# Kernel tuning notes

Hardware: AMD Instinct MI355X
Metric: run time of the kernel (lower is better)

Reference implementation:

```python
import jax, jax.numpy as jnp
import numpy as np

S, B, D, L = 100, 2048, 128, 2  # seq_len, batch, dim_model, n_layers
LN_EPS = 1e-5


def _layer_norm(x, g, b):
    # x: [S, B, D]; normalize over last dim (nn.LayerNorm(dim))
    mu = jnp.mean(x, axis=-1, keepdims=True)
    var = jnp.mean(jnp.square(x - mu), axis=-1, keepdims=True)
    return (x - mu) * jax.lax.rsqrt(var + LN_EPS) * g + b


def _asb(x, cw, cwh, thr):
    # Adaptive_Spectral_Block. x: [S, B, D] -> permute to [B, N, C]
    xb = jnp.transpose(x, (1, 0, 2)).astype(jnp.float32)  # [B, N, C]
    N = xb.shape[1]
    x_fft = jnp.fft.rfft(xb, axis=1, norm='ortho')  # [B, F, C] complex, F = N//2+1
    w = jax.lax.complex(cw[:, 0], cw[:, 1])          # [C]
    x_weighted = x_fft * w
    # adaptive high-frequency mask
    energy = jnp.sum(jnp.square(jnp.abs(x_fft)), axis=-1)  # [B, F]
    F = energy.shape[1]
    # torch.median returns the LOWER of the two middle values -> k-th smallest, k=(F-1)//2
    median = jnp.sort(energy, axis=1)[:, (F - 1) // 2][:, None]  # [B, 1]
    norm_e = energy / (median + 1e-6)
    threshold = jnp.quantile(norm_e, thr)  # global scalar quantile (linear interp, as torch)
    mask = (norm_e < threshold)[..., None].astype(x_fft.real.dtype)  # [B, F, 1]
    wh = jax.lax.complex(cwh[:, 0], cwh[:, 1])       # [C]
    x_weighted = x_weighted + (x_fft * mask) * wh
    out = jnp.fft.irfft(x_weighted, n=N, axis=1, norm='ortho')  # [B, N, C]
    return jnp.transpose(out, (1, 0, 2)).astype(x.dtype)  # back to [S, B, D]


def setup_inputs() -> dict:
    key = jax.random.key(0)
    k0, k1, k2, k3 = jax.random.split(key, 4)
    return {
        'x': jax.random.normal(k0, (S, B, D), dtype=jnp.float32),
        'complex_weight': jax.random.normal(k1, (L, D, 2), dtype=jnp.float32) * 0.02,
        'complex_weight_high': jax.random.normal(k2, (L, D, 2), dtype=jnp.float32) * 0.02,
        'threshold_param': jax.random.uniform(k3, (L,), dtype=jnp.float32) * 0.5,
        'gamma': jnp.ones((L, D), dtype=jnp.float32),
        'beta': jnp.zeros((L, D), dtype=jnp.float32),
    }


def reference(x, complex_weight, complex_weight_high, threshold_param, gamma, beta):
    # Encoder.forward: nlayers x (x = x + ASB(LayerNorm(x)))
    for i in range(L):
        h = _layer_norm(x, gamma[i], beta[i])
        x = x + _asb(h, complex_weight[i], complex_weight_high[i], threshold_param[i])
    return x
```

## Files before the change

kernel.cpp:

```cpp
#include <hip/hip_runtime.h>
#include <math.h>

#define SEQ    100
#define BATCH  2048
#define DIM    128
#define NF     51
#define NLAYER 2
#define MTOT   (BATCH * NF)
#define BD     (BATCH * DIM)
#define XSTR   16384

typedef __attribute__((ext_vector_type(8))) short bf16x8;
typedef __attribute__((ext_vector_type(4))) float f32x4v;

__device__ __forceinline__ unsigned short f2bf(float f) {
    unsigned u = __float_as_uint(f);
    return (unsigned short)((u + 0x7FFFu + ((u >> 16) & 1u)) >> 16);
}
__device__ __forceinline__ float bf2f(unsigned short u) {
    return __uint_as_float((unsigned)u << 16);
}

__global__ void k_tables(unsigned short* __restrict__ imgF,
                         unsigned short* __restrict__ imgI) {
    const int i = blockIdx.x * 256 + threadIdx.x;
    const float W = 6.28318530717958647692f / 100.f;
    if (i < 2 * 64 * 128) {
        const int p = i >> 13, k = (i >> 7) & 63, n = i & 127;
        float v = 0.f;
        if (k < NF && n < SEQ) {
            float s, c; sincosf((float)((k * n) % 100) * W, &s, &c);
            v = 0.1f * (p ? -s : c);
        }
        imgF[i] = f2bf(v);
    }
    if (i < 2 * 128 * 64) {
        const int p = i >> 13, n = (i >> 6) & 127, k = i & 63;
        float v = 0.f;
        if (k < NF && n < SEQ) {
            float s, c; sincosf((float)((k * n) % 100) * W, &s, &c);
            const float a = (k == 0 || k == 50) ? 0.1f : 0.2f;
            v = p ? -a * s : a * c;
        }
        imgI[i] = f2bf(v);
    }
}

__global__ __launch_bounds__(256, 4) void k_fwd(
    const float* __restrict__ x,
    const float* __restrict__ gamma, const float* __restrict__ beta,
    const unsigned short* __restrict__ imgF,
    unsigned short* __restrict__ Xg,
    float* __restrict__ normE)
{
    __shared__ __align__(16) unsigned short hT[128 * 128];
    __shared__ float epart[64][4];
    __shared__ float energy_s[64];
    __shared__ float med_s;

    const int b = blockIdx.x, t = threadIdx.x;
    const int lane = t & 63, wv = t >> 6, g4 = lane >> 4, cc = lane & 15;

    {
        const int c0 = lane * 2;
        const float2 gv = *(const float2*)&gamma[c0];
        const float2 bv = *(const float2*)&beta[c0];
        float2 v[4][8];
        #pragma unroll
        for (int slot = 0; slot < 4; ++slot) {
            const int n0 = (slot * 4 + wv) * 8;
            #pragma unroll
            for (int j = 0; j < 8; ++j)
                if (n0 + j < SEQ)
                    v[slot][j] = *(const float2*)&x[(size_t)(n0 + j) * BD + (size_t)b * DIM + c0];
        }
        #pragma unroll
        for (int slot = 0; slot < 4; ++slot) {
            const int chunk = slot * 4 + wv;
            const int n0 = chunk * 8;
            unsigned we[4], wo[4];
            #pragma unroll
            for (int j = 0; j < 8; ++j) {
                unsigned short he = 0, ho = 0;
                if (n0 + j < SEQ) {
                    float s  = v[slot][j].x + v[slot][j].y;
                    float s2 = fmaf(v[slot][j].x, v[slot][j].x, v[slot][j].y * v[slot][j].y);
                    #pragma unroll
                    for (int off = 1; off < 64; off <<= 1) {
                        s  += __shfl_xor(s,  off, 64);
                        s2 += __shfl_xor(s2, off, 64);
                    }
                    const float mu   = s * (1.f / 128.f);
                    const float rstd = rsqrtf(s2 * (1.f / 128.f) - mu * mu + 1e-5f);
                    he = f2bf(fmaf((v[slot][j].x - mu) * rstd, gv.x, bv.x));
                    ho = f2bf(fmaf((v[slot][j].y - mu) * rstd, gv.y, bv.y));
                }
                if (j & 1) { we[j >> 1] |= (unsigned)he << 16; wo[j >> 1] |= (unsigned)ho << 16; }
                else       { we[j >> 1]  = he;                 wo[j >> 1]  = ho; }
            }
            const int sw = (chunk ^ (lane & 7)) << 3;
            int4 ve; ve.x = (int)we[0]; ve.y = (int)we[1]; ve.z = (int)we[2]; ve.w = (int)we[3];
            int4 vo; vo.x = (int)wo[0]; vo.y = (int)wo[1]; vo.z = (int)wo[2]; vo.w = (int)wo[3];
            *(int4*)&hT[(c0    ) * 128 + sw] = ve;
            *(int4*)&hT[(c0 + 1) * 128 + sw] = vo;
        }
    }
    __syncthreads();

    bf16x8 Bf[2][4];
    #pragma unroll
    for (int ct = 0; ct < 2; ++ct) {
        const int c = wv * 32 + ct * 16 + cc;
        #pragma unroll
        for (int ks = 0; ks < 4; ++ks)
            Bf[ct][ks] = *(const bf16x8*)&hT[c * 128 + (((ks * 4 + g4) ^ (cc >> 1)) << 3)];
    }

    #pragma unroll
    for (int mt = 0; mt < 4; ++mt) {
        const int kr = mt * 16 + cc;
        f32x4v aR[2], aI[2];
        aR[0] = aR[1] = aI[0] = aI[1] = (f32x4v){0.f, 0.f, 0.f, 0.f};
        #pragma unroll
        for (int ks = 0; ks < 4; ++ks) {
            const int e0 = kr * 128 + ks * 32 + g4 * 8;
            const bf16x8 A0 = *(const bf16x8*)&imgF[e0];
            const bf16x8 A1 = *(const bf16x8*)&imgF[8192 + e0];
            #pragma unroll
            for (int ct = 0; ct < 2; ++ct) {
                aR[ct] = __builtin_amdgcn_mfma_f32_16x16x32_bf16(A0, Bf[ct][ks], aR[ct], 0, 0, 0);
                aI[ct] = __builtin_amdgcn_mfma_f32_16x16x32_bf16(A1, Bf[ct][ks], aI[ct], 0, 0, 0);
            }
        }
        #pragma unroll
        for (int reg = 0; reg < 4; ++reg) {
            float e = aR[0][reg] * aR[0][reg] + aI[0][reg] * aI[0][reg]
                    + aR[1][reg] * aR[1][reg] + aI[1][reg] * aI[1][reg];
            e += __shfl_xor(e, 1, 64); e += __shfl_xor(e, 2, 64);
            e += __shfl_xor(e, 4, 64); e += __shfl_xor(e, 8, 64);
            if (cc == 0) epart[mt * 16 + g4 * 4 + reg][wv] = e;
        }
        #pragma unroll
        for (int ct = 0; ct < 2; ++ct) {
            const int c = wv * 32 + ct * 16 + cc;
            unsigned short* Xb = Xg + (size_t)b * XSTR + (size_t)c * 128;
            const int k0 = mt * 16 + g4 * 4;
            uint2 pr, pi;
            pr.x = (unsigned)f2bf(aR[ct][0]) | ((unsigned)f2bf(aR[ct][1]) << 16);
            pr.y = (unsigned)f2bf(aR[ct][2]) | ((unsigned)f2bf(aR[ct][3]) << 16);
            pi.x = (unsigned)f2bf(aI[ct][0]) | ((unsigned)f2bf(aI[ct][1]) << 16);
            pi.y = (unsigned)f2bf(aI[ct][2]) | ((unsigned)f2bf(aI[ct][3]) << 16);
            *(uint2*)&Xb[k0]      = pr;
            *(uint2*)&Xb[64 + k0] = pi;
        }
    }
    __syncthreads();
    if (t < 64) energy_s[t] = epart[t][0] + epart[t][1] + epart[t][2] + epart[t][3];
    __syncthreads();
    if (t < NF) {
        const float e = energy_s[t];
        int cnt = 0;
        for (int j = 0; j < NF; ++j) {
            const float ej = energy_s[j];
            cnt += (ej < e || (ej == e && j < t)) ? 1 : 0;
        }
        if (cnt == (NF - 1) / 2) med_s = e;
    }
    __syncthreads();
    if (t < NF) normE[b * NF + t] = energy_s[t] / (med_s + 1e-6f);
}

__global__ void k_hist0(const float* __restrict__ normE,
                        unsigned* __restrict__ hist)
{
    __shared__ unsigned lh[2048];
    for (int i = threadIdx.x; i < 2048; i += 256) lh[i] = 0;
    __syncthreads();
    for (int i = blockIdx.x * 256 + threadIdx.x; i < MTOT; i += gridDim.x * 256)
        atomicAdd(&lh[__float_as_uint(normE[i]) >> 21], 1u);
    __syncthreads();
    for (int i = threadIdx.x; i < 2048; i += 256) {
        const unsigned c = lh[i];
        if (c) atomicAdd(&hist[i], c);
    }
}

__global__ void k_sel(const float* __restrict__ normE,
                      unsigned* __restrict__ hist,
                      unsigned* __restrict__ sel,
                      unsigned* __restrict__ done,
                      const float* __restrict__ thrp,
                      const int layer, const int phase,
                      float* __restrict__ thresh)
{
    __shared__ unsigned lh[4096];
    __shared__ unsigned sp[2], sc[2];
    __shared__ unsigned ticket_s;
    __shared__ float vb[2];
    const int t = threadIdx.x;
    const float q = thrp[layer] * (float)(MTOT - 1);
    const unsigned r0 = (unsigned)floorf(q);

    if (phase == 1) {
        if (t < 128) {
            const int j = t >> 6, ln = t & 63;
            const unsigned rk = r0 + (unsigned)j;
            unsigned sum = 0;
            for (int i = 0; i < 32; ++i) sum += hist[ln * 32 + i];
            unsigned pre = sum;
            #pragma unroll
            for (int off = 1; off < 64; off <<= 1) {
                const unsigned tt = __shfl_up(pre, off, 64);
                if (ln >= off) pre += tt;
            }
            const unsigned excl = pre - sum;
            if (rk >= excl && rk < excl + sum) {
                unsigned cum = excl;
                for (int i = 0; i < 32; ++i) {
                    const unsigned hc = hist[ln * 32 + i];
                    if (rk < cum + hc) { sp[j] = (unsigned)(ln * 32 + i) << 21; sc[j] = cum; break; }
                    cum += hc;
                }
            }
        }
    } else {
        if (t < 2) { sp[t] = sel[2 * t]; sc[t] = sel[2 * t + 1]; }
    }
    __syncthreads();
    const unsigned p0 = sp[0], p1 = sp[1];
    const int bins      = (phase == 1) ? 2048 : 1024;
    const int shift     = (phase == 1) ? 10 : 0;
    const unsigned hmsk = (phase == 1) ? 0xFFE00000u : 0xFFFFFC00u;
    const int region    = (phase == 1) ? 2048 : 6144;

    for (int i = t; i < 2 * bins; i += 256) lh[i] = 0;
    __syncthreads();
    for (int i = blockIdx.x * 256 + t; i < MTOT; i += gridDim.x * 256) {
        const unsigned v = __float_as_uint(normE[i]);
        const unsigned bin = (v >> shift) & (unsigned)(bins - 1);
        if ((v & hmsk) == p0) atomicAdd(&lh[bin], 1u);
        if ((v & hmsk) == p1) atomicAdd(&lh[bins + bin], 1u);
    }
    __syncthreads();
    for (int i = t; i < 2 * bins; i += 256) {
        const unsigned c = lh[i];
        if (c) atomicAdd(&hist[region + i], c);
    }
    __threadfence();
    if (t == 0) ticket_s = atomicAdd(&done[(layer << 1) + (phase - 1)], 1u);
    __syncthreads();
    if (ticket_s != (unsigned)(gridDim.x - 1)) return;
    __threadfence();

    if (t < 128) {
        const int j = t >> 6, ln = t & 63;
        const unsigned rk  = r0 + (unsigned)j;
        const unsigned rem = rk - sc[j];
        const unsigned* H  = hist + region + j * bins;
        const int per = bins / 64;
        unsigned sum = 0;
        for (int i = 0; i < per; ++i)
            sum += __hip_atomic_load(&H[ln * per + i], __ATOMIC_RELAXED, __HIP_MEMORY_SCOPE_AGENT);
        unsigned pre = sum;
        #pragma unroll
        for (int off = 1; off < 64; off <<= 1) {
            const unsigned tt = __shfl_up(pre, off, 64);
            if (ln >= off) pre += tt;
        }
        const unsigned excl = pre - sum;
        if (rem >= excl && rem < excl + sum) {
            unsigned cum = excl;
            for (int i = 0; i < per; ++i) {
                const unsigned hc = __hip_atomic_load(&H[ln * per + i],
                                        __ATOMIC_RELAXED, __HIP_MEMORY_SCOPE_AGENT);
                if (rem < cum + hc) {
                    const unsigned bin = (unsigned)(ln * per + i);
                    if (phase == 1) { sel[2 * j] = sp[j] | (bin << 10); sel[2 * j + 1] = sc[j] + cum; }
                    else            vb[j] = __uint_as_float(sp[j] | bin);
                    break;
                }
                cum += hc;
            }
        }
    }
    __syncthreads();
    if (phase == 1) { for (int i = t; i < 6144; i += 256) hist[i] = 0u; }
    else            { for (int i = t; i < 2048; i += 256) hist[6144 + i] = 0u; }
    if (t == 0) {
        done[(layer << 1) + (phase - 1)] = 0u;
        if (phase == 2) {
            const float frac = q - floorf(q);
            thresh[0] = vb[0] * (1.f - frac) + vb[1] * frac;
        }
    }
}

__global__ __launch_bounds__(256, 4) void k_asb(
    const float* __restrict__ x,
    const float* __restrict__ cw, const float* __restrict__ cwh,
    const unsigned short* __restrict__ Xg,
    const unsigned short* __restrict__ imgI,
    const float* __restrict__ normE, const float* __restrict__ thresh,
    float* __restrict__ out)
{
    __shared__ float mask_s[64];

    const int b = blockIdx.x, t = threadIdx.x;
    const int lane = t & 63, wv = t >> 6, g4 = lane >> 4, cc = lane & 15;

    if (t < 64) mask_s[t] = (t < NF && normE[b * NF + t] < thresh[0]) ? 1.f : 0.f;
    __syncthreads();

    bf16x8 Yr[2][2], Yi[2][2];
    #pragma unroll
    for (int ct = 0; ct < 2; ++ct) {
        const int c = wv * 32 + ct * 16 + cc;
        const unsigned short* Xb = Xg + (size_t)b * XSTR + (size_t)c * 128;
        const float2 w2 = *(const float2*)&cw[2 * c];
        const float2 h2 = *(const float2*)&cwh[2 * c];
        #pragma unroll
        for (int kb = 0; kb < 2; ++kb) {
            const bf16x8 xr = *(const bf16x8*)&Xb[kb * 32 + g4 * 8];
            const bf16x8 xi = *(const bf16x8*)&Xb[64 + kb * 32 + g4 * 8];
            bf16x8 yr, yi;
            #pragma unroll
            for (int j = 0; j < 8; ++j) {
                const float m   = mask_s[kb * 32 + g4 * 8 + j];
                const float fre = fmaf(m, h2.x, w2.x);
                const float fim = fmaf(m, h2.y, w2.y);
                const float fxr = bf2f((unsigned short)xr[j]);
                const float fxi = bf2f((unsigned short)xi[j]);
                yr[j] = (short)f2bf(fxr * fre - fxi * fim);
                yi[j] = (short)f2bf(fxr * fim + fxi * fre);
            }
            Yr[ct][kb] = yr; Yi[ct][kb] = yi;
        }
    }

    #pragma unroll
    for (int mt = 0; mt < 7; ++mt) {
        const int nr = mt * 16 + cc;
        f32x4v o[2];
        o[0] = o[1] = (f32x4v){0.f, 0.f, 0.f, 0.f};
        #pragma unroll
        for (int kb = 0; kb < 2; ++kb) {
            const int e0 = nr * 64 + kb * 32 + g4 * 8;
            const bf16x8 A0 = *(const bf16x8*)&imgI[e0];
            const bf16x8 A1 = *(const bf16x8*)&imgI[8192 + e0];
            #pragma unroll
            for (int ct = 0; ct < 2; ++ct) {
                o[ct] = __builtin_amdgcn_mfma_f32_16x16x32_bf16(A0, Yr[ct][kb], o[ct], 0, 0, 0);
                o[ct] = __builtin_amdgcn_mfma_f32_16x16x32_bf16(A1, Yi[ct][kb], o[ct], 0, 0, 0);
            }
        }
        #pragma unroll
        for (int ct = 0; ct < 2; ++ct) {
            const int c = wv * 32 + ct * 16 + cc;
            #pragma unroll
            for (int reg = 0; reg < 4; ++reg) {
                const int n = mt * 16 + g4 * 4 + reg;
                if (n < SEQ) {
                    const size_t idx = (size_t)n * BD + (size_t)b * DIM + c;
                    out[idx] = x[idx] + o[ct][reg];
                }
            }
        }
    }
}

extern "C" void kernel_launch(void* const* d_in, const int* in_sizes, int n_in,
                              void* d_out, int out_size, void* d_ws, size_t ws_size,
                              hipStream_t stream)
{
    (void)in_sizes; (void)n_in; (void)out_size; (void)ws_size;
    const float* x    = (const float*)d_in[0];
    const float* cw   = (const float*)d_in[1];
    const float* cwh  = (const float*)d_in[2];
    const float* thrp = (const float*)d_in[3];
    const float* gam  = (const float*)d_in[4];
    const float* bet  = (const float*)d_in[5];
    float* out = (float*)d_out;

    char* ws = (char*)d_ws;
    unsigned short* imgF = (unsigned short*)(ws);
    unsigned short* imgI = (unsigned short*)(ws + 32768);
    unsigned short* Xg   = (unsigned short*)(ws + 65536);
    float* normE   = (float*)(ws + 65536 + 67108864);
    unsigned* hist = (unsigned*)(ws + 65536 + 67108864 + 417792);
    unsigned* done = (unsigned*)(ws + 65536 + 67108864 + 417792 + 32768);
    unsigned* sel  = (unsigned*)(ws + 65536 + 67108864 + 417792 + 32768 + 64);
    float* thresh  = (float*)(ws + 65536 + 67108864 + 417792 + 32768 + 128);

    k_tables<<<64, 256, 0, stream>>>(imgF, imgI);
    hipMemsetAsync(hist, 0, 32768 + 64, stream);

    for (int l = 0; l < NLAYER; ++l) {
        const float* xi = (l == 0) ? x : out;
        k_fwd<<<BATCH, 256, 0, stream>>>(xi, gam + l * DIM, bet + l * DIM,
                                         imgF, Xg, normE);
        k_hist0<<<96, 256, 0, stream>>>(normE, hist);
        k_sel<<<96, 256, 0, stream>>>(normE, hist, sel, done, thrp, l, 1, thresh);
        k_sel<<<96, 256, 0, stream>>>(normE, hist, sel, done, thrp, l, 2, thresh);
        k_asb<<<BATCH, 256, 0, stream>>>(xi, cw + l * DIM * 2, cwh + l * DIM * 2,
                                         Xg, imgI, normE, thresh, out);
    }
}
```

Measured before the change: 351.6 us.

## Precompute LayerNorm stats per row, use packed bf16 converts, raise asb occupancy

LayerNorm statistics are now computed in a separate pass using 16-lane groups over float4 loads and stored in shared memory. This replaces the per-element 64-lane shuffle reductions, and x is reloaded during normalization instead of being held in registers. Software bf16 rounding is replaced with the hardware v_cvt_pk_bf16_f32 instruction in both kernels. k_asb loads its mask as vectors and its launch bounds rise to 6 blocks per SM, which may cap registers. The trade-off is that x is read twice from global memory or cache.

```diff
diff --git a/kernel.cpp b/kernel.cpp
--- a/kernel.cpp
+++ b/kernel.cpp
@@ -13,6 +13,11 @@
 typedef __attribute__((ext_vector_type(8))) short bf16x8;
 typedef __attribute__((ext_vector_type(4))) float f32x4v;
 
+__device__ __forceinline__ unsigned cvtpk(float lo, float hi) {
+    unsigned r;
+    asm("v_cvt_pk_bf16_f32 %0, %1, %2" : "=v"(r) : "v"(lo), "v"(hi));
+    return r;
+}
 __device__ __forceinline__ unsigned short f2bf(float f) {
     unsigned u = __float_as_uint(f);
     return (unsigned short)((u + 0x7FFFu + ((u >> 16) & 1u)) >> 16);
@@ -54,53 +59,78 @@
     float* __restrict__ normE)
 {
     __shared__ __align__(16) unsigned short hT[128 * 128];
+    __shared__ float2 musv[112];
     __shared__ float epart[64][4];
     __shared__ float energy_s[64];
     __shared__ float med_s;
 
     const int b = blockIdx.x, t = threadIdx.x;
     const int lane = t & 63, wv = t >> 6, g4 = lane >> 4, cc = lane & 15;
+
+    {
+        const int grp = t >> 4, ln = t & 15;
+        float4 va[7], vb[7];
+        #pragma unroll
+        for (int r = 0; r < 7; ++r) {
+            const int n = r * 16 + grp;
+            if (n < SEQ) {
+                const float* xp = &x[(size_t)n * BD + (size_t)b * DIM + ln * 8];
+                va[r] = *(const float4*)xp;
+                vb[r] = *(const float4*)(xp + 4);
+            }
+        }
+        #pragma unroll
+        for (int r = 0; r < 7; ++r) {
+            const int n = r * 16 + grp;
+            if (n < SEQ) {
+                const float4 a = va[r], c = vb[r];
+                float s  = ((a.x + a.y) + (a.z + a.w)) + ((c.x + c.y) + (c.z + c.w));
+                float s2 = fmaf(a.x, a.x, fmaf(a.y, a.y, fmaf(a.z, a.z, a.w * a.w)));
+                s2 = fmaf(c.x, c.x, fmaf(c.y, c.y, fmaf(c.z, c.z, fmaf(c.w, c.w, s2))));
+                #pragma unroll
+                for (int off = 1; off < 16; off <<= 1) {
+                    s  += __shfl_xor(s,  off, 64);
+                    s2 += __shfl_xor(s2, off, 64);
+                }
+                const float mu   = s * (1.f / 128.f);
+                const float rstd = rsqrtf(s2 * (1.f / 128.f) - mu * mu + 1e-5f);
+                if (ln == 0) musv[n] = make_float2(mu, rstd);
+            }
+        }
+    }
+    __syncthreads();
 
     {
         const int c0 = lane * 2;
         const float2 gv = *(const float2*)&gamma[c0];
         const float2 bv = *(const float2*)&beta[c0];
-        float2 v[4][8];
-        #pragma unroll
-        for (int slot = 0; slot < 4; ++slot) {
-            const int n0 = (slot * 4 + wv) * 8;
-            #pragma unroll
-            for (int j = 0; j < 8; ++j)
-                if (n0 + j < SEQ)
-                    v[slot][j] = *(const float2*)&x[(size_t)(n0 + j) * BD + (size_t)b * DIM + c0];
-        }
         #pragma unroll
         for (int slot = 0; slot < 4; ++slot) {
             const int chunk = slot * 4 + wv;
             const int n0 = chunk * 8;
-            unsigned we[4], wo[4];
+            float2 v[8]; float2 ms[8];
+            #pragma unroll
+            for (int j = 0; j < 8; ++j)
+                if (n0 + j < SEQ) {
+                    v[j]  = *(const float2*)&x[(size_t)(n0 + j) * BD + (size_t)b * DIM + c0];
+                    ms[j] = musv[n0 + j];
+                }
+            float he[8], ho[8];
             #pragma unroll
             for (int j = 0; j < 8; ++j) {
-                unsigned short he = 0, ho = 0;
+                he[j] = 0.f; ho[j] = 0.f;
                 if (n0 + j < SEQ) {
-                    float s  = v[slot][j].x + v[slot][j].y;
-                    float s2 = fmaf(v[slot][j].x, v[slot][j].x, v[slot][j].y * v[slot][j].y);
-                    #pragma unroll
-                    for (int off = 1; off < 64; off <<= 1) {
-                        s  += __shfl_xor(s,  off, 64);
-                        s2 += __shfl_xor(s2, off, 64);
-                    }
-                    const float mu   = s * (1.f / 128.f);
-                    const float rstd = rsqrtf(s2 * (1.f / 128.f) - mu * mu + 1e-5f);
-                    he = f2bf(fmaf((v[slot][j].x - mu) * rstd, gv.x, bv.x));
-                    ho = f2bf(fmaf((v[slot][j].y - mu) * rstd, gv.y, bv.y));
-                }
-                if (j & 1) { we[j >> 1] |= (unsigned)he << 16; wo[j >> 1] |= (unsigned)ho << 16; }
-                else       { we[j >> 1]  = he;                 wo[j >> 1]  = ho; }
-            }
+                    const float mb = -ms[j].x * ms[j].y;
+                    he[j] = fmaf(fmaf(v[j].x, ms[j].y, mb), gv.x, bv.x);
+                    ho[j] = fmaf(fmaf(v[j].y, ms[j].y, mb), gv.y, bv.y);
+                }
+            }
+            int4 ve, vo;
+            ve.x = (int)cvtpk(he[0], he[1]); ve.y = (int)cvtpk(he[2], he[3]);
+            ve.z = (int)cvtpk(he[4], he[5]); ve.w = (int)cvtpk(he[6], he[7]);
+            vo.x = (int)cvtpk(ho[0], ho[1]); vo.y = (int)cvtpk(ho[2], ho[3]);
+            vo.z = (int)cvtpk(ho[4], ho[5]); vo.w = (int)cvtpk(ho[6], ho[7]);
             const int sw = (chunk ^ (lane & 7)) << 3;
-            int4 ve; ve.x = (int)we[0]; ve.y = (int)we[1]; ve.z = (int)we[2]; ve.w = (int)we[3];
-            int4 vo; vo.x = (int)wo[0]; vo.y = (int)wo[1]; vo.z = (int)wo[2]; vo.w = (int)wo[3];
             *(int4*)&hT[(c0    ) * 128 + sw] = ve;
             *(int4*)&hT[(c0 + 1) * 128 + sw] = vo;
         }
@@ -146,10 +176,8 @@
             unsigned short* Xb = Xg + (size_t)b * XSTR + (size_t)c * 128;
             const int k0 = mt * 16 + g4 * 4;
             uint2 pr, pi;
-            pr.x = (unsigned)f2bf(aR[ct][0]) | ((unsigned)f2bf(aR[ct][1]) << 16);
-            pr.y = (unsigned)f2bf(aR[ct][2]) | ((unsigned)f2bf(aR[ct][3]) << 16);
-            pi.x = (unsigned)f2bf(aI[ct][0]) | ((unsigned)f2bf(aI[ct][1]) << 16);
-            pi.y = (unsigned)f2bf(aI[ct][2]) | ((unsigned)f2bf(aI[ct][3]) << 16);
+            pr.x = cvtpk(aR[ct][0], aR[ct][1]); pr.y = cvtpk(aR[ct][2], aR[ct][3]);
+            pi.x = cvtpk(aI[ct][0], aI[ct][1]); pi.y = cvtpk(aI[ct][2], aI[ct][3]);
             *(uint2*)&Xb[k0]      = pr;
             *(uint2*)&Xb[64 + k0] = pi;
         }
@@ -295,7 +323,7 @@
     }
 }
 
-__global__ __launch_bounds__(256, 4) void k_asb(
+__global__ __launch_bounds__(256, 6) void k_asb(
     const float* __restrict__ x,
     const float* __restrict__ cw, const float* __restrict__ cwh,
     const unsigned short* __restrict__ Xg,
@@ -303,13 +331,20 @@
     const float* __restrict__ normE, const float* __restrict__ thresh,
     float* __restrict__ out)
 {
-    __shared__ float mask_s[64];
+    __shared__ __align__(16) float mask_s[64];
 
     const int b = blockIdx.x, t = threadIdx.x;
     const int lane = t & 63, wv = t >> 6, g4 = lane >> 4, cc = lane & 15;
 
     if (t < 64) mask_s[t] = (t < NF && normE[b * NF + t] < thresh[0]) ? 1.f : 0.f;
     __syncthreads();
+
+    float4 mk[2][2];
+    #pragma unroll
+    for (int kb = 0; kb < 2; ++kb) {
+        mk[kb][0] = *(const float4*)&mask_s[kb * 32 + g4 * 8];
+        mk[kb][1] = *(const float4*)&mask_s[kb * 32 + g4 * 8 + 4];
+    }
 
     bf16x8 Yr[2][2], Yi[2][2];
     #pragma unroll
@@ -322,18 +357,26 @@
         for (int kb = 0; kb < 2; ++kb) {
             const bf16x8 xr = *(const bf16x8*)&Xb[kb * 32 + g4 * 8];
             const bf16x8 xi = *(const bf16x8*)&Xb[64 + kb * 32 + g4 * 8];
-            bf16x8 yr, yi;
+            float yr[8], yi[8];
             #pragma unroll
             for (int j = 0; j < 8; ++j) {
-                const float m   = mask_s[kb * 32 + g4 * 8 + j];
+                const float m   = (j < 4) ? ((const float*)&mk[kb][0])[j]
+                                          : ((const float*)&mk[kb][1])[j - 4];
                 const float fre = fmaf(m, h2.x, w2.x);
                 const float fim = fmaf(m, h2.y, w2.y);
                 const float fxr = bf2f((unsigned short)xr[j]);
                 const float fxi = bf2f((unsigned short)xi[j]);
-                yr[j] = (short)f2bf(fxr * fre - fxi * fim);
-                yi[j] = (short)f2bf(fxr * fim + fxi * fre);
-            }
-            Yr[ct][kb] = yr; Yi[ct][kb] = yi;
+                yr[j] = fxr * fre - fxi * fim;
+                yi[j] = fxr * fim + fxi * fre;
+            }
+            unsigned ur[4], ui[4];
+            #pragma unroll
+            for (int jj = 0; jj < 4; ++jj) {
+                ur[jj] = cvtpk(yr[2 * jj], yr[2 * jj + 1]);
+                ui[jj] = cvtpk(yi[2 * jj], yi[2 * jj + 1]);
+            }
+            Yr[ct][kb] = *(bf16x8*)ur;
+            Yi[ct][kb] = *(bf16x8*)ui;
         }
     }
 
```

New measurement: 382.6 us. 8.8% more time.
